# Kernel optimization log

Hardware: AMD Instinct MI355X
Metric: run time of the kernel (lower is better)

The kernel has to match this reference:

```python
import jax, jax.numpy as jnp
import numpy as np

NEG_INF = -1e9


def setup_inputs() -> dict:
    key = jax.random.key(0)
    k1, k2, k3 = jax.random.split(key, 3)
    B, C, Q, D = 32, 2048, 128, 128
    context = jax.random.normal(k1, (B, C, D), dtype=jnp.float32)
    query = jax.random.normal(k2, (B, Q, D), dtype=jnp.float32)
    # Dense(1, use_bias=False) over concat([c, q, c*q]) -> weight vector of length 3*D
    w = jax.random.normal(k3, (3 * D,), dtype=jnp.float32) * (1.0 / np.sqrt(3 * D))
    query_mask = jnp.ones((B, Q), dtype=jnp.int32)
    return {"context": context, "query": query, "w": w, "query_mask": query_mask}


def reference(context, query, w, query_mask):
    # context: [B, C, D], query: [B, Q, D], w: [3D], query_mask: [B, Q]
    D = context.shape[-1]
    w1, w2, w3 = w[:D], w[D:2 * D], w[2 * D:]
    # Trilinear similarity, exactly equal to Dense(1)(concat([c_tiled, q_tiled, c*q]))
    # S[b,c,q] = context[b,c]·w1 + query[b,q]·w2 + (context[b,c]*w3)·query[b,q]
    S = (context @ w1)[:, :, None] \
        + (query @ w2)[:, None, :] \
        + jnp.einsum('bcd,bqd->bcq', context * w3, query)  # [B, C, Q]
    mask_add = (1.0 - query_mask.astype(jnp.float32))[:, None, :] * NEG_INF
    S = S + mask_add
    a = jax.nn.softmax(S, axis=2)                  # context-to-query attention [B, C, Q]
    c2q = jnp.einsum('bcq,bqd->bcd', a, query)     # [B, C, D]
    b = jax.nn.softmax(jnp.max(S, axis=2), axis=1) # query-to-context weights [B, C]
    q2c = jnp.einsum('bc,bcd->bd', b, context)[:, None, :]  # [B, 1, D]
    q2c = jnp.broadcast_to(q2c, context.shape)     # tile over c_len
    out = jnp.concatenate([context, c2q, context * c2q, context * q2c], axis=-1)
    return out  # [B, C, 4D]
```

## Files before the change

### kernel.cpp

```cpp
#include <hip/hip_runtime.h>
#include <cstdint>

#define B_ 32
#define C_ 2048
#define Q_ 128
#define D_ 128
#define CT 64
#define OFF_ 8.0f
#define NEG_INF_F (-1.0e9f)

typedef __attribute__((ext_vector_type(8))) short bf16x8;
typedef __attribute__((ext_vector_type(4))) float f32x4;

__device__ inline short bf16_rne(float v) {
    unsigned u = __float_as_uint(v);
    return (short)((u + 0x7FFFu + ((u >> 16) & 1u)) >> 16);
}
__device__ inline void split_f32(float v, short& h, short& l) {
    unsigned u  = __float_as_uint(v);
    unsigned hb = u & 0xffff0000u;
    float lo = v - __uint_as_float(hb);
    h = (short)(hb >> 16);
    l = (short)(__float_as_uint(lo) >> 16);
}

__global__ __launch_bounds__(256)
void cqa_prep(const float* __restrict__ qry, const float* __restrict__ w,
              const int* __restrict__ qmask, float* __restrict__ qw2e_g,
              unsigned short* __restrict__ qw3Hi, unsigned short* __restrict__ qTHi)
{
    const int b = blockIdx.y, ch = blockIdx.x;
    const int t = threadIdx.x;
    const float* qb = qry + (size_t)b * Q_ * D_;

    if (t < 32) {
        int rl = t >> 1, part = t & 1;
        int q = ch * 16 + rl;
        const float* p  = qb + q * D_ + part * 64;
        const float* wp = w + D_ + part * 64;
        float s = 0.f;
        #pragma unroll
        for (int j = 0; j < 64; j += 4) {
            float4 a4 = *(const float4*)(p + j);
            float4 w4 = *(const float4*)(wp + j);
            s += a4.x*w4.x + a4.y*w4.y + a4.z*w4.z + a4.w*w4.w;
        }
        s += __shfl_xor(s, 1, 2);
        if (!part) {
            float madd = (1.0f - (float)qmask[b * Q_ + q]) * NEG_INF_F;
            qw2e_g[b * Q_ + q] = s + madd;
        }
    }
    #pragma unroll
    for (int i = 0; i < 8; ++i) {
        int idx = t + i * 256;
        int ql = idx >> 7, d = idx & 127;
        int q = ch * 16 + ql;
        float v = qb[q * D_ + d];
        qw3Hi[((size_t)b * Q_ + q) * D_ + d] = (unsigned short)bf16_rne(v * w[2 * D_ + d]);
        qTHi[((size_t)b * D_ + d) * Q_ + q]  = (unsigned short)bf16_rne(v);
    }
}

__device__ __forceinline__ void stage_b(const unsigned short* __restrict__ gH,
                                        int col0, short* sb, int wv, int lane)
{
    #pragma unroll
    for (int j = 0; j < 2; ++j) {
        int seg = wv * 2 + j;
        int li  = seg * 64 + lane;
        int row = li >> 2;
        int col = (li & 3) * 8;
        __builtin_amdgcn_global_load_lds(
            (const __attribute__((address_space(1))) void*)(gH + (size_t)row * 128 + col0 + col),
            (__attribute__((address_space(3))) void*)(sb + seg * 512), 16, 0, 0);
    }
}

__global__ __launch_bounds__(256, 4)
void cqa_main(const float* __restrict__ ctx, const float* __restrict__ w,
              const float* __restrict__ qw2e_g,
              const unsigned short* __restrict__ qw3Hi, const unsigned short* __restrict__ qTHi,
              float* __restrict__ out, float* __restrict__ part, float* __restrict__ denp_g)
{
    __shared__ __align__(16) char smem[35840];
    short* SB   = (short*)smem;
    short* PHi  = (short*)(smem + 16384);
    float* Tr   = (float*)smem;
    float* red  = (float*)smem;
    float* mlds = (float*)(smem + 33792);
    float* dred = (float*)(smem + 34048);
    float* cw1  = (float*)(smem + 34304);
    float* qw2e = (float*)(smem + 34560);

    const int b   = blockIdx.y;
    const int c0  = blockIdx.x * CT;
    const int tid = threadIdx.x;
    const int lane = tid & 63;
    const int wv   = tid >> 6;
    const int w16  = wv * 16;
    const int lm   = lane & 15;
    const int lg   = lane >> 4;
    const int lk   = lg * 8;

    const float* ctxb = ctx + ((size_t)b * C_ + c0) * D_;
    const unsigned short* qw3Hb = qw3Hi + (size_t)b * Q_ * D_;
    const unsigned short* qTHb  = qTHi + (size_t)b * Q_ * D_;

    stage_b(qw3Hb, 0, SB, wv, lane);

    if (tid < Q_) qw2e[tid] = qw2e_g[b * Q_ + tid];

    const float* arow = ctxb + (size_t)(w16 + lm) * D_;
    bf16x8 aHr[4], aLr[4];
    float cws = 0.f;
    #pragma unroll
    for (int t = 0; t < 4; ++t) {
        float4 v0 = *(const float4*)(arow + t * 32 + lk);
        float4 v1 = *(const float4*)(arow + t * 32 + lk + 4);
        float4 w0 = *(const float4*)(w + t * 32 + lk);
        float4 w1v = *(const float4*)(w + t * 32 + lk + 4);
        cws += v0.x*w0.x + v0.y*w0.y + v0.z*w0.z + v0.w*w0.w
             + v1.x*w1v.x + v1.y*w1v.y + v1.z*w1v.z + v1.w*w1v.w;
        float vv[8] = {v0.x, v0.y, v0.z, v0.w, v1.x, v1.y, v1.z, v1.w};
        #pragma unroll
        for (int i = 0; i < 8; ++i) {
            short hh, ll; split_f32(vv[i], hh, ll);
            aHr[t][i] = hh; aLr[t][i] = ll;
        }
    }
    cws += __shfl_xor(cws, 16, 64);
    cws += __shfl_xor(cws, 32, 64);
    if (lane < 16) cw1[w16 + lm] = cws;
    __syncthreads();

    float qe[8];
    #pragma unroll
    for (int f = 0; f < 8; ++f) qe[f] = qw2e[f * 16 + lm];
    float cwr[4];
    #pragma unroll
    for (int r = 0; r < 4; ++r) cwr[r] = cw1[w16 + lg * 4 + r];

    const f32x4 vzero = {0.f, 0.f, 0.f, 0.f};
    f32x4 acc[8];
    #pragma unroll
    for (int f = 0; f < 8; ++f) acc[f] = vzero;

    #pragma unroll
    for (int t = 0; t < 4; ++t) {
        if (t < 3) stage_b(qw3Hb, (t + 1) * 32, SB + ((t + 1) & 1) * 4096, wv, lane);
        else       stage_b(qTHb,  0,            SB,                        wv, lane);
        const short* sb = SB + (t & 1) * 4096;
        bf16x8 aH = aHr[t], aL = aLr[t];
        #pragma unroll
        for (int f = 0; f < 8; ++f) {
            bf16x8 bH = *(const bf16x8*)(sb + (f * 16 + lm) * 32 + lk);
            acc[f] = __builtin_amdgcn_mfma_f32_16x16x32_bf16(aH, bH, acc[f], 0, 0, 0);
            acc[f] = __builtin_amdgcn_mfma_f32_16x16x32_bf16(aL, bH, acc[f], 0, 0, 0);
        }
        __syncthreads();
    }

    float inv[4];
    #pragma unroll
    for (int r = 0; r < 4; ++r) {
        float sv[8];
        float mx = -3.0e38f;
        #pragma unroll
        for (int f = 0; f < 8; ++f) {
            sv[f] = acc[f][r] + qe[f];
            mx = fmaxf(mx, sv[f]);
        }
        mx = fmaxf(mx, __shfl_xor(mx, 1, 16));
        mx = fmaxf(mx, __shfl_xor(mx, 2, 16));
        mx = fmaxf(mx, __shfl_xor(mx, 4, 16));
        mx = fmaxf(mx, __shfl_xor(mx, 8, 16));
        int lrow = w16 + lg * 4 + r;
        float s = 0.f;
        #pragma unroll
        for (int f = 0; f < 8; ++f) {
            float p = __expf(sv[f] - mx);
            s += p;
            PHi[lrow * 136 + f * 16 + lm] = bf16_rne(p);
        }
        s += __shfl_xor(s, 1, 16);
        s += __shfl_xor(s, 2, 16);
        s += __shfl_xor(s, 4, 16);
        s += __shfl_xor(s, 8, 16);
        inv[r] = 1.0f / s;
        if (lm == 0) mlds[lrow] = mx + cwr[r];
    }

    f32x4 acc2[8];
    #pragma unroll
    for (int f = 0; f < 8; ++f) acc2[f] = vzero;

    #pragma unroll
    for (int t = 0; t < 4; ++t) {
        if (t < 3) stage_b(qTHb, (t + 1) * 32, SB + ((t + 1) & 1) * 4096, wv, lane);
        const short* sb = SB + (t & 1) * 4096;
        bf16x8 aH = *(const bf16x8*)(PHi + (w16 + lm) * 136 + t * 32 + lk);
        #pragma unroll
        for (int f = 0; f < 8; ++f) {
            bf16x8 bH = *(const bf16x8*)(sb + (f * 16 + lm) * 32 + lk);
            acc2[f] = __builtin_amdgcn_mfma_f32_16x16x32_bf16(aH, bH, acc2[f], 0, 0, 0);
        }
        __syncthreads();
    }

    #pragma unroll
    for (int r = 0; r < 4; ++r) {
        int lrow = w16 + lg * 4 + r;
        #pragma unroll
        for (int f = 0; f < 8; ++f)
            Tr[lrow * 132 + f * 16 + lm] = acc2[f][r] * inv[r];
    }
    __syncthreads();

    const int rsel = tid >> 5;
    const int dd   = (tid & 31) * 4;
    float4 qacc = {0.f, 0.f, 0.f, 0.f};
    float denp = 0.f;
    #pragma unroll
    for (int pass = 0; pass < 8; ++pass) {
        int row = pass * 8 + rsel;
        float4 a  = *(const float4*)(Tr + row * 132 + dd);
        float4 cv = *(const float4*)(ctxb + (size_t)row * D_ + dd);
        float wgt = __expf(mlds[row] - OFF_);
        size_t obase = ((size_t)b * C_ + c0 + row) * (4 * D_);
        float4 p;
        p.x = cv.x*a.x; p.y = cv.y*a.y; p.z = cv.z*a.z; p.w = cv.w*a.w;
        *(float4*)(out + obase + dd)          = cv;
        *(float4*)(out + obase + D_ + dd)     = a;
        *(float4*)(out + obase + 2 * D_ + dd) = p;
        qacc.x += wgt * cv.x; qacc.y += wgt * cv.y;
        qacc.z += wgt * cv.z; qacc.w += wgt * cv.w;
        denp += wgt;
    }
    __syncthreads();
    *(float4*)(red + rsel * 128 + dd) = qacc;
    if ((tid & 31) == 0) dred[rsel] = denp;
    __syncthreads();
    if (tid < 128) {
        float s = 0.f;
        #pragma unroll
        for (int rr = 0; rr < 8; ++rr) s += red[rr * 128 + tid];
        part[((size_t)b * 32 + blockIdx.x) * 128 + tid] = s;
    }
    if (tid == 0) {
        float s = 0.f;
        #pragma unroll
        for (int rr = 0; rr < 8; ++rr) s += dred[rr];
        denp_g[b * 32 + blockIdx.x] = s;
    }
}

__global__ __launch_bounds__(128)
void cqa_q2c(const float* __restrict__ part, const float* __restrict__ denp_g,
             float* __restrict__ q2c)
{
    int b = blockIdx.x, d = threadIdx.x;
    float den = 0.f;
    #pragma unroll
    for (int j = 0; j < 32; ++j) den += denp_g[b * 32 + j];
    float s = 0.f;
    #pragma unroll
    for (int j = 0; j < 32; ++j) s += part[((size_t)b * 32 + j) * 128 + d];
    q2c[b * 128 + d] = s / den;
}

__global__ __launch_bounds__(256)
void cqa_out4(const float* __restrict__ ctx, const float* __restrict__ q2c,
              float* __restrict__ out)
{
    size_t i = (size_t)blockIdx.x * 256 + threadIdx.x;
    const size_t n4 = (size_t)B_*C_*D_/4;
    if (i >= n4) return;
    size_t bc = i >> 5;
    int d4 = (int)(i & 31);
    int b  = (int)(bc >> 11);
    float4 c4 = reinterpret_cast<const float4*>(ctx)[i];
    float4 g4 = reinterpret_cast<const float4*>(q2c)[b*32 + d4];
    float4 o;
    o.x = c4.x*g4.x; o.y = c4.y*g4.y; o.z = c4.z*g4.z; o.w = c4.w*g4.w;
    reinterpret_cast<float4*>(out)[bc*128 + 96 + d4] = o;
}

extern "C" void kernel_launch(void* const* d_in, const int* in_sizes, int n_in,
                              void* d_out, int out_size, void* d_ws, size_t ws_size,
                              hipStream_t stream)
{
    const float* ctx   = (const float*)d_in[0];
    const float* qry   = (const float*)d_in[1];
    const float* w     = (const float*)d_in[2];
    const int*   qmask = (const int*)d_in[3];
    float* out = (float*)d_out;
    float* ws  = (float*)d_ws;

    float* part    = ws;
    float* denp_g  = ws + 131072;
    float* q2c     = ws + 132096;
    float* qw2e_g  = ws + 136192;
    unsigned short* bf = (unsigned short*)(ws + 140288);
    unsigned short* qw3Hi = bf;
    unsigned short* qTHi  = bf + 524288;

    cqa_prep<<<dim3(8, B_), 256, 0, stream>>>(qry, w, qmask, qw2e_g, qw3Hi, qTHi);
    cqa_main<<<dim3(C_/CT, B_), 256, 0, stream>>>(ctx, w, qw2e_g, qw3Hi, qTHi,
                                                  out, part, denp_g);
    cqa_q2c<<<B_, 128, 0, stream>>>(part, denp_g, q2c);
    cqa_out4<<<(int)(((size_t)B_*C_*D_/4 + 255)/256), 256, 0, stream>>>(ctx, q2c, out);
}
```

Measured before the change: 53.95 us.

## Transpose second GEMM to read query fragments from global and shrink LDS

The second GEMM (P·Q) is reorganised so each wave loads its query (qT) A-fragments straight from global memory into registers, and reads the probability tile from LDS as the B operand. That removes the qT staging loop and its barriers. LDS shrinks from about 35.8KB to 27KB by reusing the P buffer as the second stage buffer, and launch bounds rise to 6 blocks per CU. The transposed output goes through LDS in two half passes. This adds global fragment loads and extra synchronisation, and raises register pressure under the tighter occupancy bound.

```diff
diff --git a/kernel.cpp b/kernel.cpp
--- a/kernel.cpp
+++ b/kernel.cpp
@@ -77,21 +77,22 @@
     }
 }
 
-__global__ __launch_bounds__(256, 4)
+__global__ __launch_bounds__(256, 6)
 void cqa_main(const float* __restrict__ ctx, const float* __restrict__ w,
               const float* __restrict__ qw2e_g,
               const unsigned short* __restrict__ qw3Hi, const unsigned short* __restrict__ qTHi,
               float* __restrict__ out, float* __restrict__ part, float* __restrict__ denp_g)
 {
-    __shared__ __align__(16) char smem[35840];
+    __shared__ __align__(16) char smem[27008];
     short* SB   = (short*)smem;
-    short* PHi  = (short*)(smem + 16384);
+    short* PHi  = (short*)(smem + 8192);
     float* Tr   = (float*)smem;
     float* red  = (float*)smem;
-    float* mlds = (float*)(smem + 33792);
-    float* dred = (float*)(smem + 34048);
-    float* cw1  = (float*)(smem + 34304);
-    float* qw2e = (float*)(smem + 34560);
+    float* mlds = (float*)(smem + 25600);
+    float* slds = (float*)(smem + 25856);
+    float* cw1  = (float*)(smem + 26112);
+    float* qw2e = (float*)(smem + 26368);
+    float* dred = (float*)(smem + 26880);
 
     const int b   = blockIdx.y;
     const int c0  = blockIdx.x * CT;
@@ -148,9 +149,8 @@
 
     #pragma unroll
     for (int t = 0; t < 4; ++t) {
-        if (t < 3) stage_b(qw3Hb, (t + 1) * 32, SB + ((t + 1) & 1) * 4096, wv, lane);
-        else       stage_b(qTHb,  0,            SB,                        wv, lane);
-        const short* sb = SB + (t & 1) * 4096;
+        if (t < 3) stage_b(qw3Hb, (t + 1) * 32, ((t + 1) & 1) ? PHi : SB, wv, lane);
+        const short* sb = (t & 1) ? PHi : SB;
         bf16x8 aH = aHr[t], aL = aLr[t];
         #pragma unroll
         for (int f = 0; f < 8; ++f) {
@@ -161,7 +161,13 @@
         __syncthreads();
     }
 
-    float inv[4];
+    bf16x8 qa[2][4];
+    #pragma unroll
+    for (int ds = 0; ds < 2; ++ds)
+        #pragma unroll
+        for (int t = 0; t < 4; ++t)
+            qa[ds][t] = *(const bf16x8*)(qTHb + (size_t)(ds * 64 + w16 + lm) * 128 + t * 32 + lk);
+
     #pragma unroll
     for (int r = 0; r < 4; ++r) {
         float sv[8];
@@ -187,33 +193,24 @@
         s += __shfl_xor(s, 2, 16);
         s += __shfl_xor(s, 4, 16);
         s += __shfl_xor(s, 8, 16);
-        inv[r] = 1.0f / s;
-        if (lm == 0) mlds[lrow] = mx + cwr[r];
-    }
-
-    f32x4 acc2[8];
-    #pragma unroll
-    for (int f = 0; f < 8; ++f) acc2[f] = vzero;
+        if (lm == 0) { mlds[lrow] = mx + cwr[r]; slds[lrow] = 1.0f / s; }
+    }
+    __syncthreads();
+
+    f32x4 acc2[2][4];
+    #pragma unroll
+    for (int ds = 0; ds < 2; ++ds)
+        #pragma unroll
+        for (int fc = 0; fc < 4; ++fc) acc2[ds][fc] = vzero;
 
     #pragma unroll
     for (int t = 0; t < 4; ++t) {
-        if (t < 3) stage_b(qTHb, (t + 1) * 32, SB + ((t + 1) & 1) * 4096, wv, lane);
-        const short* sb = SB + (t & 1) * 4096;
-        bf16x8 aH = *(const bf16x8*)(PHi + (w16 + lm) * 136 + t * 32 + lk);
-        #pragma unroll
-        for (int f = 0; f < 8; ++f) {
-            bf16x8 bH = *(const bf16x8*)(sb + (f * 16 + lm) * 32 + lk);
-            acc2[f] = __builtin_amdgcn_mfma_f32_16x16x32_bf16(aH, bH, acc2[f], 0, 0, 0);
-        }
-        __syncthreads();
-    }
-
-    #pragma unroll
-    for (int r = 0; r < 4; ++r) {
-        int lrow = w16 + lg * 4 + r;
-        #pragma unroll
-        for (int f = 0; f < 8; ++f)
-            Tr[lrow * 132 + f * 16 + lm] = acc2[f][r] * inv[r];
+        #pragma unroll
+        for (int fc = 0; fc < 4; ++fc) {
+            bf16x8 bP = *(const bf16x8*)(PHi + (fc * 16 + lm) * 136 + t * 32 + lk);
+            acc2[0][fc] = __builtin_amdgcn_mfma_f32_16x16x32_bf16(qa[0][t], bP, acc2[0][fc], 0, 0, 0);
+            acc2[1][fc] = __builtin_amdgcn_mfma_f32_16x16x32_bf16(qa[1][t], bP, acc2[1][fc], 0, 0, 0);
+        }
     }
     __syncthreads();
 
@@ -222,22 +219,41 @@
     float4 qacc = {0.f, 0.f, 0.f, 0.f};
     float denp = 0.f;
     #pragma unroll
-    for (int pass = 0; pass < 8; ++pass) {
-        int row = pass * 8 + rsel;
-        float4 a  = *(const float4*)(Tr + row * 132 + dd);
-        float4 cv = *(const float4*)(ctxb + (size_t)row * D_ + dd);
-        float wgt = __expf(mlds[row] - OFF_);
-        size_t obase = ((size_t)b * C_ + c0 + row) * (4 * D_);
-        float4 p;
-        p.x = cv.x*a.x; p.y = cv.y*a.y; p.z = cv.z*a.z; p.w = cv.w*a.w;
-        *(float4*)(out + obase + dd)          = cv;
-        *(float4*)(out + obase + D_ + dd)     = a;
-        *(float4*)(out + obase + 2 * D_ + dd) = p;
-        qacc.x += wgt * cv.x; qacc.y += wgt * cv.y;
-        qacc.z += wgt * cv.z; qacc.w += wgt * cv.w;
-        denp += wgt;
-    }
-    __syncthreads();
+    for (int p = 0; p < 2; ++p) {
+        #pragma unroll
+        for (int fq = 0; fq < 2; ++fq) {
+            int fc = 2 * p + fq;
+            float ic = slds[fc * 16 + lm];
+            int cl = fq * 16 + lm;
+            #pragma unroll
+            for (int ds = 0; ds < 2; ++ds) {
+                f32x4 v = acc2[ds][fc];
+                float4 o;
+                o.x = v[0] * ic; o.y = v[1] * ic; o.z = v[2] * ic; o.w = v[3] * ic;
+                *(float4*)(Tr + cl * 132 + ds * 64 + w16 + lg * 4) = o;
+            }
+        }
+        __syncthreads();
+        #pragma unroll
+        for (int i = 0; i < 4; ++i) {
+            int cl  = i * 8 + rsel;
+            int row = p * 32 + cl;
+            float4 a  = *(const float4*)(Tr + cl * 132 + dd);
+            float4 cv = *(const float4*)(ctxb + (size_t)row * D_ + dd);
+            float wgt = __expf(mlds[row] - OFF_);
+            size_t obase = ((size_t)b * C_ + c0 + row) * (4 * D_);
+            float4 pr;
+            pr.x = cv.x*a.x; pr.y = cv.y*a.y; pr.z = cv.z*a.z; pr.w = cv.w*a.w;
+            *(float4*)(out + obase + dd)          = cv;
+            *(float4*)(out + obase + D_ + dd)     = a;
+            *(float4*)(out + obase + 2 * D_ + dd) = pr;
+            qacc.x += wgt * cv.x; qacc.y += wgt * cv.y;
+            qacc.z += wgt * cv.z; qacc.w += wgt * cv.w;
+            denp += wgt;
+        }
+        __syncthreads();
+    }
+
     *(float4*)(red + rsel * 128 + dd) = qacc;
     if ((tid & 31) == 0) dred[rsel] = denp;
     __syncthreads();
```

Measured after the change: 71.15 us. +31.9%, slower.
